# Kernel tuning notes

Hardware: AMD Instinct MI355X
Metric: run time of the kernel (lower is better)

## Reference

```python
import jax, jax.numpy as jnp
import numpy as np

EMBED_DIM = 1024
FFN_DIM = 4096
N_QUBITS = 16
BATCH, SEQ = 4, 2048


def setup_inputs() -> dict:
    key = jax.random.key(0)
    ks = jax.random.split(key, 6)
    s1 = 1.0 / np.sqrt(EMBED_DIM)
    s2 = 1.0 / np.sqrt(FFN_DIM)
    s3 = 1.0 / np.sqrt(N_QUBITS)
    return {
        "x": jax.random.normal(ks[0], (BATCH, SEQ, EMBED_DIM), jnp.float32),
        "W1": jax.random.normal(ks[1], (FFN_DIM, EMBED_DIM), jnp.float32) * s1,
        "Wq": jax.random.normal(ks[2], (N_QUBITS, FFN_DIM), jnp.float32) * s2,
        "theta": jax.random.normal(ks[3], (N_QUBITS,), jnp.float32),
        "W2": jax.random.normal(ks[4], (FFN_DIM, N_QUBITS), jnp.float32) * s3,
        "Wo": jax.random.normal(ks[5], (EMBED_DIM, FFN_DIM), jnp.float32) * s2,
    }


def reference(x, W1, Wq, theta, W2, Wo):
    # linear1: [b,s,e] @ [f,e]^T -> [b,s,f]
    h = jnp.einsum('bse,fe->bsf', x, W1)
    # to_qubits: [b,s,f] -> [b,s,q]
    q = jnp.einsum('bsf,qf->bsq', h, Wq)
    # Quantum circuit: RX(q_i) encoding then trainable RX(theta_i) per wire,
    # wires are unentangled product states -> <Z_i> = cos(q_i + theta_i).
    qm = jnp.cos(q + theta)
    # linear2 + relu
    h2 = jax.nn.relu(jnp.einsum('bsq,fq->bsf', qm, W2))
    # out_proj (dropout is identity in eval / p=0)
    return jnp.einsum('bsf,ef->bse', h2, Wo)
```

## Files before the change

### kernel.cpp

```cpp
#include <hip/hip_runtime.h>
#include <hip/hip_bf16.h>
#include <math.h>

typedef _Float16 f16;
typedef __attribute__((ext_vector_type(8))) _Float16 f16x8;
typedef __attribute__((ext_vector_type(4))) _Float16 f16x4;
typedef __attribute__((ext_vector_type(4))) float f32x4;

#define M_TOT 8192
#define E_DIM 1024
#define F_DIM 4096
#define NQ    16

#define BARRIER() asm volatile("s_barrier" ::: "memory")
#define WAITV(n)  asm volatile("s_waitcnt vmcnt(" #n ")" ::: "memory")
#define WAITLGKM() asm volatile("s_waitcnt lgkmcnt(0)" ::: "memory")

__device__ __forceinline__ f16x8 cvt8(float4 a, float4 b) {
    f16x8 o;
    o[0] = (f16)a.x; o[1] = (f16)a.y; o[2] = (f16)a.z; o[3] = (f16)a.w;
    o[4] = (f16)b.x; o[5] = (f16)b.y; o[6] = (f16)b.z; o[7] = (f16)b.w;
    return o;
}

__global__ __launch_bounds__(256) void prep_kernel(
    const float* __restrict__ W1, f16* __restrict__ W1t,
    const float* __restrict__ wo, f16* __restrict__ woh,
    const float* __restrict__ W2, f16* __restrict__ w2p)
{
    __shared__ float ls[64][68];
    const int b = blockIdx.x;
    if (b < 1024) {
        const int bf = b & 63;
        const int be = b >> 6;
        const int t  = threadIdx.x;
        const int r  = t >> 4;
        const int c4 = (t & 15) * 4;
        #pragma unroll
        for (int i = 0; i < 4; ++i) {
            int fr = r + i * 16;
            float4 v = *reinterpret_cast<const float4*>(W1 + (size_t)(bf * 64 + fr) * E_DIM + be * 64 + c4);
            ls[fr][c4] = v.x; ls[fr][c4 + 1] = v.y; ls[fr][c4 + 2] = v.z; ls[fr][c4 + 3] = v.w;
        }
        __syncthreads();
        const int er = t >> 2;
        const int fc = (t & 3) * 16;
        f16x8 o0, o1;
        #pragma unroll
        for (int j = 0; j < 8; ++j) { o0[j] = (f16)ls[fc + j][er]; o1[j] = (f16)ls[fc + 8 + j][er]; }
        f16* dst = W1t + (size_t)(be * 64 + er) * F_DIM + bf * 64 + fc;
        *reinterpret_cast<f16x8*>(dst)     = o0;
        *reinterpret_cast<f16x8*>(dst + 8) = o1;
    } else if (b < 3072) {
        size_t i = ((size_t)(b - 1024) * 256 + threadIdx.x) * 8;
        float4 v0 = *reinterpret_cast<const float4*>(wo + i);
        float4 v1 = *reinterpret_cast<const float4*>(wo + i + 4);
        *reinterpret_cast<f16x8*>(woh + i) = cvt8(v0, v1);
    } else {
        int t = (b - 3072) * 256 + threadIdx.x;
        size_t i = (size_t)t * 8;
        int col = (int)(i & 31);
        f16x8 o;
        if (col < NQ) {
            int row = (int)(i >> 5);
            float4 v0 = *reinterpret_cast<const float4*>(W2 + (size_t)row * NQ + col);
            float4 v1 = *reinterpret_cast<const float4*>(W2 + (size_t)row * NQ + col + 4);
            o = cvt8(v0, v1);
        } else {
            for (int k = 0; k < 8; ++k) o[k] = (f16)0.f;
        }
        *reinterpret_cast<f16x8*>(w2p + i) = o;
    }
}

__global__ __launch_bounds__(256) void tg_kernel(
    const float* __restrict__ Wq, const f16* __restrict__ W1t,
    float* __restrict__ pT)
{
    const int w = threadIdx.x >> 6, lane = threadIdx.x & 63;
    const int fr = lane & 15, fq = lane >> 4;
    const int kc = blockIdx.x & 15;
    const int et = blockIdx.x >> 4;
    const int e0 = et * 128 + w * 32;
    const int kbase = kc * 256;

    f32x4 acc[2] = {};
    #pragma unroll
    for (int s = 0; s < 8; ++s) {
        int k = kbase + s * 32 + fq * 8;
        float4 a0 = *reinterpret_cast<const float4*>(Wq + (size_t)fr * F_DIM + k);
        float4 a1 = *reinterpret_cast<const float4*>(Wq + (size_t)fr * F_DIM + k + 4);
        f16x8 af = cvt8(a0, a1);
        #pragma unroll
        for (int n = 0; n < 2; ++n) {
            f16x8 bf = *reinterpret_cast<const f16x8*>(W1t + (size_t)(e0 + n * 16 + fr) * F_DIM + k);
            acc[n] = __builtin_amdgcn_mfma_f32_16x16x32_f16(af, bf, acc[n], 0, 0, 0);
        }
    }
    #pragma unroll
    for (int n = 0; n < 2; ++n)
        #pragma unroll
        for (int j = 0; j < 4; ++j)
            pT[(size_t)kc * (16 * E_DIM) + (size_t)(fq * 4 + j) * E_DIM + e0 + n * 16 + fr] = acc[n][j];
}

__global__ __launch_bounds__(256) void treduce_kernel(
    const float* __restrict__ pT, f16* __restrict__ Th)
{
    int idx = blockIdx.x * 256 + threadIdx.x;
    float s = 0.f;
    #pragma unroll
    for (int kc = 0; kc < 16; ++kc) s += pT[(size_t)kc * (16 * E_DIM) + idx];
    Th[idx] = (f16)s;
}

__global__ __launch_bounds__(256) void qx_kernel(
    const float* __restrict__ x, const f16* __restrict__ Th,
    float* __restrict__ pq2)
{
    __shared__ __align__(16) f16 ths[16 * 512];
    const int tid = threadIdx.x, w = tid >> 6, lane = tid & 63;
    const int fr = lane & 15, fq = lane >> 4;
    const int kc = blockIdx.x & 1;
    const int m0 = (blockIdx.x >> 1) * 64;

    #pragma unroll
    for (int i = 0; i < 4; ++i) {
        int tau = i * 256 + tid;
        int q   = tau >> 6;
        int kb  = tau & 63;
        f16x8 v = *reinterpret_cast<const f16x8*>(Th + (size_t)q * E_DIM + kc * 512 + kb * 8);
        int boff = (q * 1024 + kb * 16) ^ ((q & 7) << 4);
        *reinterpret_cast<f16x8*>((char*)ths + boff) = v;
    }
    __syncthreads();

    const int row = m0 + w * 16 + fr;
    const float* xa = x + (size_t)row * E_DIM + kc * 512;
    f32x4 acc = {};
    #pragma unroll
    for (int s = 0; s < 16; ++s) {
        int ko = s * 32 + fq * 8;
        float4 a0 = *reinterpret_cast<const float4*>(xa + ko);
        float4 a1 = *reinterpret_cast<const float4*>(xa + ko + 4);
        f16x8 af = cvt8(a0, a1);
        int boff = (fr * 1024 + ko * 2) ^ ((fr & 7) << 4);
        f16x8 bf = *reinterpret_cast<const f16x8*>((char*)ths + boff);
        acc = __builtin_amdgcn_mfma_f32_16x16x32_f16(af, bf, acc, 0, 0, 0);
    }
    #pragma unroll
    for (int j = 0; j < 4; ++j)
        pq2[(size_t)kc * (M_TOT * NQ) + (size_t)(m0 + w * 16 + fq * 4 + j) * NQ + fr] = acc[j];
}

__global__ __launch_bounds__(256) void qfinal_kernel(
    const float* __restrict__ pq2, const float* __restrict__ theta,
    f16* __restrict__ qmp)
{
    int t = blockIdx.x * 256 + threadIdx.x;
    int row = t >> 4, q = t & 15;
    float s = pq2[t] + pq2[(size_t)M_TOT * NQ + t];
    float v = cosf(s + theta[q]);
    qmp[(size_t)row * 32 + q]      = (f16)v;
    qmp[(size_t)row * 32 + 16 + q] = (f16)0.f;
}

__device__ __forceinline__ void gload_lds16(const f16* g, f16* l) {
    __builtin_amdgcn_global_load_lds(
        (const __attribute__((address_space(1))) void*)(g),
        (__attribute__((address_space(3))) void*)(l), 16, 0, 0);
}

__global__ __launch_bounds__(512, 2)
void gemm4f(const f16* __restrict__ qmp, const f16* __restrict__ w2p,
            const f16* __restrict__ Wo, f16* __restrict__ P0, f16* __restrict__ P1)
{
    extern __shared__ __align__(16) f16 smem[];
    const int tid  = threadIdx.x;
    const int w    = tid >> 6;
    const int lane = tid & 63;

    const int nwg = gridDim.x;
    const int bid = blockIdx.x;
    const int cpx = nwg >> 3;
    int swz = (bid & 7) * cpx + (bid >> 3);
    const int per = nwg >> 1;
    const int split = swz / per;
    const int r = swz % per;
    const int by = r >> 2, bx = r & 3;
    const int m0 = by * 256, n0 = bx * 256;

    const int wr = w >> 2, wc = w & 3;
    const int fr = lane & 15, fq = lane >> 4;
    const int K = 2048;

    const f16* Bb  = Wo + (size_t)split * K;
    const f16* w2g = w2p + (size_t)split * K * 32;
    f16* Pout = split ? P1 : P0;

    const int r0w = w * 32 + fr;
    f16x8 qreg0 = *reinterpret_cast<const f16x8*>(qmp + (size_t)(m0 + r0w) * 32 + fq * 8);
    f16x8 qreg1 = *reinterpret_cast<const f16x8*>(qmp + (size_t)(m0 + r0w + 16) * 32 + fq * 8);

    const int rl   = w * 8 + (lane >> 3);
    const int scol = (((lane & 7) ^ (rl & 7)) * 8);
    const f16* gB = Bb + (size_t)(n0 + rl) * F_DIM + scol;
    f16* lB = smem + 16384 + w * 512;

#define SB(b,h,j,kt) gload_lds16(gB + (size_t)((h)*128 + (j)*64) * F_DIM + (kt), lB + (b)*32768 + (h)*8192 + (j)*4096)
#define SBH(b,h,kt) do { SB(b,h,0,kt); SB(b,h,1,kt); } while(0)

    f16x8 w2a[4], w2b[4];
#define LOADW2(R, kt) do { _Pragma("unroll") \
    for (int ft = 0; ft < 4; ++ft) \
        R[ft] = *reinterpret_cast<const f16x8*>(w2g + (size_t)((kt) + ft*16 + fr) * 32 + fq * 8); } while(0)

#define PRODUCE(bdst, W2R) do {                                                   \
    f32x4 z_ = {0.f, 0.f, 0.f, 0.f};                                              \
    _Pragma("unroll") for (int ft = 0; ft < 4; ++ft) {                            \
        f32x4 c0_ = __builtin_amdgcn_mfma_f32_16x16x32_f16(W2R[ft], qreg0, z_, 0, 0, 0); \
        f32x4 c1_ = __builtin_amdgcn_mfma_f32_16x16x32_f16(W2R[ft], qreg1, z_, 0, 0, 0); \
        f16x4 h0_, h1_;                                                           \
        _Pragma("unroll") for (int jj = 0; jj < 4; ++jj) {                        \
            h0_[jj] = (f16)fmaxf(c0_[jj], 0.f); h1_[jj] = (f16)fmaxf(c1_[jj], 0.f); } \
        const int sl_ = (2 * ft + (fq >> 1)) ^ (fr & 7);                          \
        *reinterpret_cast<f16x4*>(smem + (bdst)*32768 + (r0w)*64      + sl_*8 + ((fq & 1) << 2)) = h0_; \
        *reinterpret_cast<f16x4*>(smem + (bdst)*32768 + (r0w+16)*64   + sl_*8 + ((fq & 1) << 2)) = h1_; \
    } } while(0)

    const int xm  = fr & 7;
    const int so0 = ((0 + fq) ^ xm) * 8;
    const int so1 = ((4 + fq) ^ xm) * 8;
    const int aro = (wr * 128 + fr) * 64;
    const int bro = (wc * 64  + fr) * 64;

#define AF(b,m,ks) (*reinterpret_cast<const f16x8*>(smem + (b)*32768 + aro + (m)*1024 + so##ks))
#define BF(b,n,ks) (*reinterpret_cast<const f16x8*>(smem + (b)*32768 + 16384 + bro + (n)*1024 + so##ks))

    f32x4 acc[8][4] = {};
    f16x8 bf[4][2];

#define PHASE(b, p, STAGES, W4) do {                                              \
    f16x8 a00 = AF(b, 2*(p),   0), a01 = AF(b, 2*(p),   1);                       \
    f16x8 a10 = AF(b, 2*(p)+1, 0), a11 = AF(b, 2*(p)+1, 1);                       \
    if ((p) == 0) { _Pragma("unroll")                                             \
        for (int n = 0; n < 4; ++n) { bf[n][0] = BF(b,n,0); bf[n][1] = BF(b,n,1); } } \
    STAGES;                                                                       \
    BARRIER();                                                                    \
    __builtin_amdgcn_s_setprio(1);                                                \
    _Pragma("unroll") for (int n = 0; n < 4; ++n) {                               \
        acc[2*(p)  ][n] = __builtin_amdgcn_mfma_f32_16x16x32_f16(a00, bf[n][0], acc[2*(p)  ][n], 0,0,0); \
        acc[2*(p)+1][n] = __builtin_amdgcn_mfma_f32_16x16x32_f16(a10, bf[n][0], acc[2*(p)+1][n], 0,0,0); } \
    _Pragma("unroll") for (int n = 0; n < 4; ++n) {                               \
        acc[2*(p)  ][n] = __builtin_amdgcn_mfma_f32_16x16x32_f16(a01, bf[n][1], acc[2*(p)  ][n], 0,0,0); \
        acc[2*(p)+1][n] = __builtin_amdgcn_mfma_f32_16x16x32_f16(a11, bf[n][1], acc[2*(p)+1][n], 0,0,0); } \
    __builtin_amdgcn_s_setprio(0);                                                \
    if (W4) { WAITV(8); WAITLGKM(); }                                             \
    BARRIER(); } while(0)

    const int NT = K >> 6;
    const int NI = NT >> 1;

    LOADW2(w2b, 0);
    LOADW2(w2a, 64);
    SBH(0,0,0);  SBH(0,1,0);
    SBH(1,0,64); SBH(1,1,64);
    WAITV(0);
    BARRIER();
    PRODUCE(0, w2b);
    WAITLGKM();
    BARRIER();

    for (int i = 0; i < NI; ++i) {
        const int k1 = (2*i+1) << 6;
        int t2 = 2*i+2; if (t2 > NT-1) t2 = NT-1;
        int t3 = 2*i+3; if (t3 > NT-1) t3 = NT-1;
        const int k2 = t2 << 6, k3 = t3 << 6;
        PHASE(0, 0, PRODUCE(1, w2a),            0);
        PHASE(0, 1, LOADW2(w2b, k2); SBH(0,0,k2), 0);
        PHASE(0, 2, SBH(0,1,k2),                0);
        PHASE(0, 3, ,                           1);
        PHASE(1, 0, PRODUCE(0, w2b),            0);
        PHASE(1, 1, LOADW2(w2a, k3); SBH(1,0,k3), 0);
        PHASE(1, 2, SBH(1,1,k3),                0);
        PHASE(1, 3, ,                           1);
    }
    WAITV(0);

    #pragma unroll
    for (int m = 0; m < 8; ++m) {
        #pragma unroll
        for (int n = 0; n < 4; ++n) {
            #pragma unroll
            for (int j = 0; j < 4; ++j) {
                int row = m0 + wr * 128 + m * 16 + fq * 4 + j;
                int col = n0 + wc * 64  + n * 16 + fr;
                Pout[(size_t)row * E_DIM + col] = (f16)acc[m][n][j];
            }
        }
    }
#undef SB
#undef SBH
#undef LOADW2
#undef PRODUCE
#undef AF
#undef BF
#undef PHASE
}

__global__ __launch_bounds__(256) void out_reduce2_kernel(
    float* __restrict__ out, const f16* __restrict__ p0, const f16* __restrict__ p1)
{
    size_t i = ((size_t)blockIdx.x * 256 + threadIdx.x) * 8;
    f16x8 a = *reinterpret_cast<const f16x8*>(p0 + i);
    f16x8 b = *reinterpret_cast<const f16x8*>(p1 + i);
    float4 v0, v1;
    v0.x = (float)a[0] + (float)b[0]; v0.y = (float)a[1] + (float)b[1];
    v0.z = (float)a[2] + (float)b[2]; v0.w = (float)a[3] + (float)b[3];
    v1.x = (float)a[4] + (float)b[4]; v1.y = (float)a[5] + (float)b[5];
    v1.z = (float)a[6] + (float)b[6]; v1.w = (float)a[7] + (float)b[7];
    *reinterpret_cast<float4*>(out + i)     = v0;
    *reinterpret_cast<float4*>(out + i + 4) = v1;
}

extern "C" void kernel_launch(void* const* d_in, const int* in_sizes, int n_in,
                              void* d_out, int out_size, void* d_ws, size_t ws_size,
                              hipStream_t stream) {
    const float* x  = (const float*)d_in[0];
    const float* W1 = (const float*)d_in[1];
    const float* Wq = (const float*)d_in[2];
    const float* th = (const float*)d_in[3];
    const float* W2 = (const float*)d_in[4];
    const float* Wo = (const float*)d_in[5];
    float* out = (float*)d_out;

    char* base = (char*)d_ws;
    float* pT  = (float*)base;
    f16*   Th  = (f16*)(base + (1 << 20));
    float* pq2 = (float*)(base + (1 << 20) + (1 << 16));
    f16*   w1t = (f16*)(base + 16777216);
    f16*   woh = w1t + (size_t)E_DIM * F_DIM;
    f16*   w2p = woh + (size_t)E_DIM * F_DIM;
    f16*   qmp = w2p + (size_t)F_DIM * 32;
    f16*   p0  = qmp + (size_t)M_TOT * 32;
    f16*   p1  = p0  + (size_t)M_TOT * E_DIM;

    static bool attr_done = false;
    if (!attr_done) {
        hipFuncSetAttribute((const void*)&gemm4f,
                            hipFuncAttributeMaxDynamicSharedMemorySize, 131072);
        attr_done = true;
    }

    prep_kernel<<<3136, 256, 0, stream>>>(W1, w1t, Wo, woh, W2, w2p);
    tg_kernel<<<128, 256, 0, stream>>>(Wq, w1t, pT);
    treduce_kernel<<<64, 256, 0, stream>>>(pT, Th);
    qx_kernel<<<256, 256, 0, stream>>>(x, Th, pq2);
    qfinal_kernel<<<512, 256, 0, stream>>>(pq2, th, qmp);
    gemm4f<<<256, 512, 131072, stream>>>(qmp, w2p, woh, p0, p1);
    out_reduce2_kernel<<<4096, 256, 0, stream>>>(out, p0, p1);
}
```

Baseline: 115.1 us.

## Fuse qx and cosine finalize into one kernel; interleave producer MFMAs with main GEMM

Merges the split-K q projection and the cosine finalize into a single kernel. Each 512-thread block computes both K halves and reduces them through LDS, which removes one launch and the pq2 global round trip. In the main GEMM, the W2/relu producer MFMAs are issued in the same high-priority region as the phase-0 main MFMAs, and their LDS writes are deferred until after them, so the producer work can overlap with the main matrix math. The risks are halved grid parallelism for the q kernel (128 blocks) and extra register pressure in gemm4f from holding eight producer accumulators live.

Result: no change. 116.9 us (+1.6%).

```diff
diff --git a/kernel.cpp b/kernel.cpp
--- a/kernel.cpp
+++ b/kernel.cpp
@@ -114,29 +114,30 @@
     Th[idx] = (f16)s;
 }
 
-__global__ __launch_bounds__(256) void qx_kernel(
+__global__ __launch_bounds__(512) void qx2_kernel(
     const float* __restrict__ x, const f16* __restrict__ Th,
-    float* __restrict__ pq2)
-{
-    __shared__ __align__(16) f16 ths[16 * 512];
+    const float* __restrict__ theta, f16* __restrict__ qmp)
+{
+    __shared__ __align__(16) f16 ths[16 * 1024];
+    __shared__ float pql[2048];
     const int tid = threadIdx.x, w = tid >> 6, lane = tid & 63;
     const int fr = lane & 15, fq = lane >> 4;
-    const int kc = blockIdx.x & 1;
-    const int m0 = (blockIdx.x >> 1) * 64;
+    const int m0 = blockIdx.x * 64;
 
     #pragma unroll
     for (int i = 0; i < 4; ++i) {
-        int tau = i * 256 + tid;
-        int q   = tau >> 6;
-        int kb  = tau & 63;
-        f16x8 v = *reinterpret_cast<const f16x8*>(Th + (size_t)q * E_DIM + kc * 512 + kb * 8);
-        int boff = (q * 1024 + kb * 16) ^ ((q & 7) << 4);
+        int tau = i * 512 + tid;
+        int q   = tau >> 7;
+        int kb  = tau & 127;
+        f16x8 v = *reinterpret_cast<const f16x8*>(Th + (size_t)q * E_DIM + kb * 8);
+        int boff = (q * 2048 + kb * 16) ^ ((q & 7) << 4);
         *reinterpret_cast<f16x8*>((char*)ths + boff) = v;
     }
     __syncthreads();
 
-    const int row = m0 + w * 16 + fr;
-    const float* xa = x + (size_t)row * E_DIM + kc * 512;
+    const int kc = w >> 2;
+    const int rg = w & 3;
+    const float* xa = x + (size_t)(m0 + rg * 16 + fr) * E_DIM + kc * 512;
     f32x4 acc = {};
     #pragma unroll
     for (int s = 0; s < 16; ++s) {
@@ -144,25 +145,24 @@
         float4 a0 = *reinterpret_cast<const float4*>(xa + ko);
         float4 a1 = *reinterpret_cast<const float4*>(xa + ko + 4);
         f16x8 af = cvt8(a0, a1);
-        int boff = (fr * 1024 + ko * 2) ^ ((fr & 7) << 4);
+        int boff = (fr * 2048 + (kc * 512 + ko) * 2) ^ ((fr & 7) << 4);
         f16x8 bf = *reinterpret_cast<const f16x8*>((char*)ths + boff);
         acc = __builtin_amdgcn_mfma_f32_16x16x32_f16(af, bf, acc, 0, 0, 0);
     }
     #pragma unroll
     for (int j = 0; j < 4; ++j)
-        pq2[(size_t)kc * (M_TOT * NQ) + (size_t)(m0 + w * 16 + fq * 4 + j) * NQ + fr] = acc[j];
-}
-
-__global__ __launch_bounds__(256) void qfinal_kernel(
-    const float* __restrict__ pq2, const float* __restrict__ theta,
-    f16* __restrict__ qmp)
-{
-    int t = blockIdx.x * 256 + threadIdx.x;
-    int row = t >> 4, q = t & 15;
-    float s = pq2[t] + pq2[(size_t)M_TOT * NQ + t];
-    float v = cosf(s + theta[q]);
-    qmp[(size_t)row * 32 + q]      = (f16)v;
-    qmp[(size_t)row * 32 + 16 + q] = (f16)0.f;
+        pql[(kc * 64 + rg * 16 + fq * 4 + j) * 16 + fr] = acc[j];
+    __syncthreads();
+
+    #pragma unroll
+    for (int e = 0; e < 2; ++e) {
+        int idx = e * 512 + tid;
+        int row = idx >> 4, q = idx & 15;
+        float s = pql[idx] + pql[1024 + idx];
+        float v = cosf(s + theta[q]);
+        qmp[(size_t)(m0 + row) * 32 + q]      = (f16)v;
+        qmp[(size_t)(m0 + row) * 32 + 16 + q] = (f16)0.f;
+    }
 }
 
 __device__ __forceinline__ void gload_lds16(const f16* g, f16* l) {
@@ -215,17 +215,21 @@
     for (int ft = 0; ft < 4; ++ft) \
         R[ft] = *reinterpret_cast<const f16x8*>(w2g + (size_t)((kt) + ft*16 + fr) * 32 + fq * 8); } while(0)
 
+#define PWRITE(bdst, ft, C0, C1) do {                                             \
+    f16x4 h0_, h1_;                                                               \
+    _Pragma("unroll") for (int jj = 0; jj < 4; ++jj) {                            \
+        h0_[jj] = (f16)fmaxf(C0[jj], 0.f); h1_[jj] = (f16)fmaxf(C1[jj], 0.f); }   \
+    const int sl_ = (2 * (ft) + (fq >> 1)) ^ (fr & 7);                            \
+    *reinterpret_cast<f16x4*>(smem + (bdst)*32768 + (r0w)*64    + sl_*8 + ((fq & 1) << 2)) = h0_; \
+    *reinterpret_cast<f16x4*>(smem + (bdst)*32768 + (r0w+16)*64 + sl_*8 + ((fq & 1) << 2)) = h1_; \
+    } while(0)
+
 #define PRODUCE(bdst, W2R) do {                                                   \
     f32x4 z_ = {0.f, 0.f, 0.f, 0.f};                                              \
     _Pragma("unroll") for (int ft = 0; ft < 4; ++ft) {                            \
         f32x4 c0_ = __builtin_amdgcn_mfma_f32_16x16x32_f16(W2R[ft], qreg0, z_, 0, 0, 0); \
         f32x4 c1_ = __builtin_amdgcn_mfma_f32_16x16x32_f16(W2R[ft], qreg1, z_, 0, 0, 0); \
-        f16x4 h0_, h1_;                                                           \
-        _Pragma("unroll") for (int jj = 0; jj < 4; ++jj) {                        \
-            h0_[jj] = (f16)fmaxf(c0_[jj], 0.f); h1_[jj] = (f16)fmaxf(c1_[jj], 0.f); } \
-        const int sl_ = (2 * ft + (fq >> 1)) ^ (fr & 7);                          \
-        *reinterpret_cast<f16x4*>(smem + (bdst)*32768 + (r0w)*64      + sl_*8 + ((fq & 1) << 2)) = h0_; \
-        *reinterpret_cast<f16x4*>(smem + (bdst)*32768 + (r0w+16)*64   + sl_*8 + ((fq & 1) << 2)) = h1_; \
+        PWRITE(bdst, ft, c0_, c1_);                                               \
     } } while(0)
 
     const int xm  = fr & 7;
@@ -239,6 +243,14 @@
 
     f32x4 acc[8][4] = {};
     f16x8 bf[4][2];
+
+#define MAINMMA(p, a00, a01, a10, a11)                                            \
+    _Pragma("unroll") for (int n = 0; n < 4; ++n) {                               \
+        acc[2*(p)  ][n] = __builtin_amdgcn_mfma_f32_16x16x32_f16(a00, bf[n][0], acc[2*(p)  ][n], 0,0,0); \
+        acc[2*(p)+1][n] = __builtin_amdgcn_mfma_f32_16x16x32_f16(a10, bf[n][0], acc[2*(p)+1][n], 0,0,0); } \
+    _Pragma("unroll") for (int n = 0; n < 4; ++n) {                               \
+        acc[2*(p)  ][n] = __builtin_amdgcn_mfma_f32_16x16x32_f16(a01, bf[n][1], acc[2*(p)  ][n], 0,0,0); \
+        acc[2*(p)+1][n] = __builtin_amdgcn_mfma_f32_16x16x32_f16(a11, bf[n][1], acc[2*(p)+1][n], 0,0,0); }
 
 #define PHASE(b, p, STAGES, W4) do {                                              \
     f16x8 a00 = AF(b, 2*(p),   0), a01 = AF(b, 2*(p),   1);                       \
@@ -248,14 +260,31 @@
     STAGES;                                                                       \
     BARRIER();                                                                    \
     __builtin_amdgcn_s_setprio(1);                                                \
-    _Pragma("unroll") for (int n = 0; n < 4; ++n) {                               \
-        acc[2*(p)  ][n] = __builtin_amdgcn_mfma_f32_16x16x32_f16(a00, bf[n][0], acc[2*(p)  ][n], 0,0,0); \
-        acc[2*(p)+1][n] = __builtin_amdgcn_mfma_f32_16x16x32_f16(a10, bf[n][0], acc[2*(p)+1][n], 0,0,0); } \
-    _Pragma("unroll") for (int n = 0; n < 4; ++n) {                               \
-        acc[2*(p)  ][n] = __builtin_amdgcn_mfma_f32_16x16x32_f16(a01, bf[n][1], acc[2*(p)  ][n], 0,0,0); \
-        acc[2*(p)+1][n] = __builtin_amdgcn_mfma_f32_16x16x32_f16(a11, bf[n][1], acc[2*(p)+1][n], 0,0,0); } \
+    MAINMMA(p, a00, a01, a10, a11);                                               \
     __builtin_amdgcn_s_setprio(0);                                                \
     if (W4) { WAITV(8); WAITLGKM(); }                                             \
+    BARRIER(); } while(0)
+
+#define PHASEP(b, bdst, W2R) do {                                                 \
+    f16x8 a00 = AF(b, 0, 0), a01 = AF(b, 0, 1);                                   \
+    f16x8 a10 = AF(b, 1, 0), a11 = AF(b, 1, 1);                                   \
+    _Pragma("unroll")                                                             \
+    for (int n = 0; n < 4; ++n) { bf[n][0] = BF(b,n,0); bf[n][1] = BF(b,n,1); }   \
+    BARRIER();                                                                    \
+    __builtin_amdgcn_s_setprio(1);                                                \
+    f32x4 z_ = {0.f, 0.f, 0.f, 0.f};                                              \
+    f32x4 c00 = __builtin_amdgcn_mfma_f32_16x16x32_f16(W2R[0], qreg0, z_, 0,0,0); \
+    f32x4 c10 = __builtin_amdgcn_mfma_f32_16x16x32_f16(W2R[0], qreg1, z_, 0,0,0); \
+    f32x4 c01 = __builtin_amdgcn_mfma_f32_16x16x32_f16(W2R[1], qreg0, z_, 0,0,0); \
+    f32x4 c11 = __builtin_amdgcn_mfma_f32_16x16x32_f16(W2R[1], qreg1, z_, 0,0,0); \
+    f32x4 c02 = __builtin_amdgcn_mfma_f32_16x16x32_f16(W2R[2], qreg0, z_, 0,0,0); \
+    f32x4 c12 = __builtin_amdgcn_mfma_f32_16x16x32_f16(W2R[2], qreg1, z_, 0,0,0); \
+    f32x4 c03 = __builtin_amdgcn_mfma_f32_16x16x32_f16(W2R[3], qreg0, z_, 0,0,0); \
+    f32x4 c13 = __builtin_amdgcn_mfma_f32_16x16x32_f16(W2R[3], qreg1, z_, 0,0,0); \
+    MAINMMA(0, a00, a01, a10, a11);                                               \
+    __builtin_amdgcn_s_setprio(0);                                                \
+    PWRITE(bdst, 0, c00, c10); PWRITE(bdst, 1, c01, c11);                         \
+    PWRITE(bdst, 2, c02, c12); PWRITE(bdst, 3, c03, c13);                         \
     BARRIER(); } while(0)
 
     const int NT = K >> 6;
@@ -272,15 +301,14 @@
     BARRIER();
 
     for (int i = 0; i < NI; ++i) {
-        const int k1 = (2*i+1) << 6;
         int t2 = 2*i+2; if (t2 > NT-1) t2 = NT-1;
         int t3 = 2*i+3; if (t3 > NT-1) t3 = NT-1;
         const int k2 = t2 << 6, k3 = t3 << 6;
-        PHASE(0, 0, PRODUCE(1, w2a),            0);
+        PHASEP(0, 1, w2a);
         PHASE(0, 1, LOADW2(w2b, k2); SBH(0,0,k2), 0);
         PHASE(0, 2, SBH(0,1,k2),                0);
         PHASE(0, 3, ,                           1);
-        PHASE(1, 0, PRODUCE(0, w2b),            0);
+        PHASEP(1, 0, w2b);
         PHASE(1, 1, LOADW2(w2a, k3); SBH(1,0,k3), 0);
         PHASE(1, 2, SBH(1,1,k3),                0);
         PHASE(1, 3, ,                           1);
@@ -302,10 +330,13 @@
 #undef SB
 #undef SBH
 #undef LOADW2
+#undef PWRITE
 #undef PRODUCE
 #undef AF
 #undef BF
+#undef MAINMMA
 #undef PHASE
+#undef PHASEP
 }
 
 __global__ __launch_bounds__(256) void out_reduce2_kernel(
@@ -337,7 +368,6 @@
     char* base = (char*)d_ws;
     float* pT  = (float*)base;
     f16*   Th  = (f16*)(base + (1 << 20));
-    float* pq2 = (float*)(base + (1 << 20) + (1 << 16));
     f16*   w1t = (f16*)(base + 16777216);
     f16*   woh = w1t + (size_t)E_DIM * F_DIM;
     f16*   w2p = woh + (size_t)E_DIM * F_DIM;
@@ -355,8 +385,7 @@
     prep_kernel<<<3136, 256, 0, stream>>>(W1, w1t, Wo, woh, W2, w2p);
     tg_kernel<<<128, 256, 0, stream>>>(Wq, w1t, pT);
     treduce_kernel<<<64, 256, 0, stream>>>(pT, Th);
-    qx_kernel<<<256, 256, 0, stream>>>(x, Th, pq2);
-    qfinal_kernel<<<512, 256, 0, stream>>>(pq2, th, qmp);
+    qx2_kernel<<<128, 512, 0, stream>>>(x, Th, th, qmp);
     gemm4f<<<256, 512, 131072, stream>>>(qmp, w2p, woh, p0, p1);
     out_reduce2_kernel<<<4096, 256, 0, stream>>>(out, p0, p1);
 }
```
